# Optimization experiments

Hardware: AMD Instinct MI355X
Metric: run time of the kernel (lower is better)

Reference implementation:

```python
import jax, jax.numpy as jnp
import numpy as np
from jax import lax

NGTH = 15  # num_gth_mem
EPS = 1e-5  # BatchNorm eps


def _conv(x, w, b):
    y = lax.conv_general_dilated(x, w, (1, 1), 'VALID',
                                 dimension_numbers=('NCHW', 'OIHW', 'NCHW'))
    return y + b[None, :, None, None]


def _bn(x, g, b, m, v):
    # eval-mode BatchNorm2d with running stats
    return g[None, :, None, None] * (x - m[None, :, None, None]) * lax.rsqrt(v[None, :, None, None] + EPS) + b[None, :, None, None]


def _masked_stats(x, w):
    # x: (B, M, ...) ; w: (B, M) float weights. Population mean/std over masked mem slots.
    extra = (1,) * (x.ndim - 2)
    we = w.reshape(w.shape[:2] + extra)
    cnt = jnp.sum(w, axis=1).reshape((w.shape[0],) + extra)
    s = jnp.sum(x * we, axis=1)
    ss = jnp.sum(x * x * we, axis=1)
    mean = s / cnt
    var = jnp.maximum(ss / cnt - mean * mean, 0.0)
    return mean, jnp.sqrt(var)


def _forward(target_scores, ptm, pmt, predicted_iou, mem_mask, params):
    nf, ns, nmem, c, h, w = ptm.shape
    B = nf * ns
    ts = target_scores.reshape(B, 1, h, w)
    pmt = pmt.reshape(B, nmem, 1, h, w)
    ptm = ptm.reshape(B, nmem, c, h, w)
    mask = mem_mask.reshape(B, nmem)
    piou = predicted_iou.reshape(B, 1, 1, 1)

    mf = mask.astype(ts.dtype)
    # rank of each selected slot within the masked (ordered) selection
    rank = jnp.cumsum(mf, axis=1) - 1.0
    gth_w = mf * (rank < NGTH).astype(ts.dtype)   # first NGTH selected slots
    oth_w = mf * (rank >= NGTH).astype(ts.dtype)  # remaining selected slots

    max_ts = jnp.max(ts.reshape(B, -1), axis=1)

    pmt_mean, pmt_std = _masked_stats(pmt, mf)                 # (B,1,h,w)
    pmt_gth = pmt[:, :NGTH]                                    # unmasked slice (as in torch code)
    pmt_gth_mean = jnp.mean(pmt_gth, axis=1)
    pmt_gth_std = jnp.std(pmt_gth, axis=1)
    pmt_oth_mean, pmt_oth_std = _masked_stats(pmt, oth_w)

    ptm_max = jnp.max(ptm.reshape(B, nmem, -1), axis=2)        # (B, nmem)
    m_mm, s_mm = _masked_stats(ptm_max, mf)
    m_gm, s_gm = _masked_stats(ptm_max, gth_w)
    m_om, s_om = _masked_stats(ptm_max, oth_w)

    def bcast(v):
        return jnp.broadcast_to(v.reshape(B, 1, 1, 1), (B, 1, h, w))

    inp = jnp.concatenate([
        bcast(max_ts), jnp.broadcast_to(piou, (B, 1, h, w)),
        pmt_mean, pmt_std, pmt_gth_mean, pmt_gth_std, pmt_oth_mean, pmt_oth_std,
        bcast(m_mm), bcast(s_mm), bcast(m_gm), bcast(s_gm), bcast(m_om), bcast(s_om)
    ], axis=1)  # (B, 14, h, w)

    (c1w, c1b, g1, b1, m1, v1, c2w, c2b, g2, b2, m2, v2,
     c3w, c3b, g3, b3, m3, v3, c4w, c4b) = params
    x = jax.nn.relu(_bn(_conv(inp, c1w, c1b), g1, b1, m1, v1))
    x = lax.reduce_window(x, -jnp.inf, lax.max, (1, 1, 2, 2), (1, 1, 2, 2), 'VALID')
    x = jax.nn.relu(_bn(_conv(x, c2w, c2b), g2, b2, m2, v2))
    x = jax.nn.relu(_bn(_conv(x, c3w, c3b), g3, b3, m3, v3))
    x = _conv(x, c4w, c4b)
    return jnp.max(x, axis=(2, 3), keepdims=True)  # AdaptiveMaxPool2d((1,1)) -> (B,1,1,1)


def setup_inputs() -> dict:
    key = jax.random.key(0)
    ks = jax.random.split(key, 16)
    nf, ns, nmem, h, w = 16, 32, 30, 32, 32
    d = {}
    d['target_scores'] = jax.random.normal(ks[0], (nf, ns, 1, h, w), jnp.float32)
    d['ptm'] = jax.random.uniform(ks[1], (nf, ns, nmem, 1, h, w), jnp.float32)
    d['pmt'] = jax.random.uniform(ks[2], (nf, ns, nmem, 1, h, w), jnp.float32)
    d['predicted_iou'] = jax.random.uniform(ks[3], (nf, ns), jnp.float32)
    mask = jax.random.uniform(ks[4], (nf, ns, nmem)) < 0.7
    mask = mask.at[..., :20].set(True)  # >= 20 selected -> 'other' set non-empty
    d['mem_mask'] = mask
    d['conv1_w'] = jax.random.normal(ks[5], (64, 14, 3, 3), jnp.float32) * 0.1
    d['conv1_b'] = jnp.zeros((64,), jnp.float32)
    d['bn1_g'] = jnp.ones((64,), jnp.float32); d['bn1_b'] = jnp.zeros((64,), jnp.float32)
    d['bn1_m'] = jnp.zeros((64,), jnp.float32); d['bn1_v'] = jnp.ones((64,), jnp.float32)
    d['conv2_w'] = jax.random.normal(ks[6], (64, 64, 3, 3), jnp.float32) * 0.05
    d['conv2_b'] = jnp.zeros((64,), jnp.float32)
    d['bn2_g'] = jnp.ones((64,), jnp.float32); d['bn2_b'] = jnp.zeros((64,), jnp.float32)
    d['bn2_m'] = jnp.zeros((64,), jnp.float32); d['bn2_v'] = jnp.ones((64,), jnp.float32)
    d['conv3_w'] = jax.random.normal(ks[7], (64, 64, 3, 3), jnp.float32) * 0.05
    d['conv3_b'] = jnp.zeros((64,), jnp.float32)
    d['bn3_g'] = jnp.ones((64,), jnp.float32); d['bn3_b'] = jnp.zeros((64,), jnp.float32)
    d['bn3_m'] = jnp.zeros((64,), jnp.float32); d['bn3_v'] = jnp.ones((64,), jnp.float32)
    d['conv4_w'] = jax.random.normal(ks[8], (1, 64, 3, 3), jnp.float32) * 0.05
    d['conv4_b'] = jnp.zeros((1,), jnp.float32)
    return d


def reference(target_scores, ptm, pmt, predicted_iou, mem_mask,
              conv1_w, conv1_b, bn1_g, bn1_b, bn1_m, bn1_v,
              conv2_w, conv2_b, bn2_g, bn2_b, bn2_m, bn2_v,
              conv3_w, conv3_b, bn3_g, bn3_b, bn3_m, bn3_v,
              conv4_w, conv4_b):
    params = (conv1_w, conv1_b, bn1_g, bn1_b, bn1_m, bn1_v,
              conv2_w, conv2_b, bn2_g, bn2_b, bn2_m, bn2_v,
              conv3_w, conv3_b, bn3_g, bn3_b, bn3_m, bn3_v,
              conv4_w, conv4_b)
    return _forward(target_scores, ptm, pmt, predicted_iou, mem_mask, params)
```

## Files before the change

kernel.cpp:

```cpp
#include <hip/hip_runtime.h>
#include <math.h>

#define NFB  512
#define NMEM 30
#define PIX  1024
#define EPSF 1e-5f

typedef _Float16 half8_t __attribute__((ext_vector_type(8)));
typedef _Float16 half4_t __attribute__((ext_vector_type(4)));
typedef float float4_t __attribute__((ext_vector_type(4)));

#define OFF_W2R   13631488
#define OFF_W3R   13705216
#define OFF_WR1   13778944
#define OFF_WSUM1 13791232

__global__ __launch_bounds__(256) void k_prep(
    const float* __restrict__ c1w, const float* __restrict__ c2w,
    const float* __restrict__ c3w, _Float16* __restrict__ w2rep,
    _Float16* __restrict__ w3rep, _Float16* __restrict__ wr1,
    float* __restrict__ wsum1)
{
  int i = blockIdx.x * 256 + threadIdx.x;
  if (i < 36864) {
    int kr = i / 12288, rem = i - kr * 12288;
    int oc = rem / 192, k = rem - oc * 192;
    int kc = k >> 6, ci = k & 63;
    w2rep[i] = (_Float16)c2w[((oc * 64 + ci) * 3 + kr) * 3 + kc];
  } else if (i < 73728) {
    int j = i - 36864;
    int kr = j / 12288, rem = j - kr * 12288;
    int oc = rem / 192, k = rem - oc * 192;
    int kc = k >> 6, ci = k & 63;
    w3rep[j] = (_Float16)c3w[((oc * 64 + ci) * 3 + kr) * 3 + kc];
  } else if (i < 79872) {
    int j = i - 73728;
    int kr = j / 2048, rem = j - kr * 2048;
    int oc = rem >> 5, k = rem & 31;
    int kc = k >> 3, ci = k & 7;
    _Float16 v = (_Float16)0.f;
    if (kc < 3 && ci < 6)
      v = (_Float16)c1w[((oc * 14 + (2 + ci)) * 3 + kr) * 3 + kc];
    wr1[j] = v;
  } else if (i < 80384) {
    int j = i - 79872;
    int oc = j >> 3, u = j & 7;
    const int uch[8] = {0, 1, 8, 9, 10, 11, 12, 13};
    const float* wp = c1w + (oc * 14 + uch[u]) * 9;
    float s = 0.f;
    #pragma unroll
    for (int k = 0; k < 9; ++k) s += wp[k];
    wsum1[j] = s;
  }
}

__global__ __launch_bounds__(256, 2) void k_mega(
    const float* __restrict__ ts, const float* __restrict__ ptm,
    const float* __restrict__ pmt, const float* __restrict__ piou,
    const int* __restrict__ mask,
    const _Float16* __restrict__ wr1, const float* __restrict__ wsum1,
    const float* __restrict__ c1b, const float* __restrict__ g1,
    const float* __restrict__ b1, const float* __restrict__ m1,
    const float* __restrict__ v1,
    const _Float16* __restrict__ w2rep,
    const float* __restrict__ c2b, const float* __restrict__ g2,
    const float* __restrict__ b2, const float* __restrict__ m2,
    const float* __restrict__ v2,
    const _Float16* __restrict__ w3rep,
    const float* __restrict__ c3b, const float* __restrict__ g3,
    const float* __restrict__ b3, const float* __restrict__ m3,
    const float* __restrict__ v3,
    const float* __restrict__ c4w, const float* __restrict__ c4b,
    _Float16* __restrict__ x2h, float* __restrict__ out)
{
  __shared__ __align__(16) char s_buf[55296];
  __shared__ float s_wm[NMEM], s_wo[NMEM], s_pmax[NMEM];
  __shared__ float s_red[4], s_scal[12], s_cnt[4];
  __shared__ float s_w4[576];

  const int b = blockIdx.x, t = threadIdx.x;
  const int lane = t & 63, wave = t >> 6;
  const int n16 = lane & 15, q = lane >> 4;
  _Float16* const IMG = (_Float16*)s_buf;
  _Float16* const X1  = (_Float16*)(s_buf + 16448);
  _Float16* const X2S = (_Float16*)s_buf;
  _Float16* const X3  = (_Float16*)(s_buf + 29952);

  for (int i = t; i < 576; i += 256) {
    int ci = i / 9, k = i - ci * 9;
    s_w4[k * 64 + ci] = c4w[i];
  }
  if (t == 0) {
    float cum = 0.f, cm = 0.f, cg = 0.f, co = 0.f;
    for (int m = 0; m < NMEM; ++m) {
      float f  = (mask[b * NMEM + m] != 0) ? 1.f : 0.f;
      float gg = (cum < 15.f) ? f : 0.f;
      float oo = f - gg;
      cum += f;
      s_wm[m] = f; s_wo[m] = oo;
      cm += f; cg += gg; co += oo;
    }
    s_cnt[0] = cm; s_cnt[1] = cg; s_cnt[2] = co;
  }
  for (int m = wave; m < NMEM; m += 4) {
    const float* p = ptm + ((size_t)b * NMEM + m) * PIX;
    float4 v0 = *(const float4*)(p + lane * 4);
    float4 v1_ = *(const float4*)(p + lane * 4 + 256);
    float4 v2_ = *(const float4*)(p + lane * 4 + 512);
    float4 v3_ = *(const float4*)(p + lane * 4 + 768);
    float mx = fmaxf(fmaxf(fmaxf(v0.x, v0.y), fmaxf(v0.z, v0.w)),
                     fmaxf(fmaxf(v1_.x, v1_.y), fmaxf(v1_.z, v1_.w)));
    mx = fmaxf(mx, fmaxf(fmaxf(fmaxf(v2_.x, v2_.y), fmaxf(v2_.z, v2_.w)),
                         fmaxf(fmaxf(v3_.x, v3_.y), fmaxf(v3_.z, v3_.w))));
    #pragma unroll
    for (int off = 32; off > 0; off >>= 1)
      mx = fmaxf(mx, __shfl_down(mx, off, 64));
    if (lane == 0) s_pmax[m] = mx;
  }
  {
    float4 v = ((const float4*)(ts + (size_t)b * PIX))[t];
    float mx = fmaxf(fmaxf(v.x, v.y), fmaxf(v.z, v.w));
    #pragma unroll
    for (int off = 32; off > 0; off >>= 1)
      mx = fmaxf(mx, __shfl_down(mx, off, 64));
    if (lane == 0) s_red[wave] = mx;
  }
  __syncthreads();
  if (t == 0) {
    float maxts = fmaxf(fmaxf(s_red[0], s_red[1]), fmaxf(s_red[2], s_red[3]));
    float sm = 0, sm2 = 0, sg = 0, sg2 = 0, so = 0, so2 = 0;
    for (int m = 0; m < NMEM; ++m) {
      float x = s_pmax[m];
      float gg = s_wm[m] - s_wo[m];
      sm += s_wm[m] * x;  sm2 += s_wm[m] * x * x;
      sg += gg * x;       sg2 += gg * x * x;
      so += s_wo[m] * x;  so2 += s_wo[m] * x * x;
    }
    float cm = s_cnt[0], cg = s_cnt[1], co = s_cnt[2];
    float a = sm / cm, g = sg / cg, o = so / co;
    s_scal[0] = maxts; s_scal[1] = piou[b];
    s_scal[2] = a; s_scal[3] = sqrtf(fmaxf(sm2 / cm - a * a, 0.f));
    s_scal[4] = g; s_scal[5] = sqrtf(fmaxf(sg2 / cg - g * g, 0.f));
    s_scal[6] = o; s_scal[7] = sqrtf(fmaxf(so2 / co - o * o, 0.f));
  }
  {
    const float cm = s_cnt[0], co = s_cnt[2];
    const int p0 = t * 4;
    const float* pb = pmt + (size_t)b * NMEM * PIX + p0;
    float sA[4] = {0,0,0,0}, qA[4] = {0,0,0,0};
    float sG[4] = {0,0,0,0}, qG[4] = {0,0,0,0};
    float sO[4] = {0,0,0,0}, qO[4] = {0,0,0,0};
    #pragma unroll 1
    for (int mb = 0; mb < 15; mb += 5) {
      float4 v[5];
      #pragma unroll
      for (int j = 0; j < 5; ++j) v[j] = *(const float4*)(pb + (size_t)(mb + j) * PIX);
      #pragma unroll
      for (int j = 0; j < 5; ++j) {
        float wm = s_wm[mb + j], wo = s_wo[mb + j];
        float xv[4] = {v[j].x, v[j].y, v[j].z, v[j].w};
        #pragma unroll
        for (int k = 0; k < 4; ++k) {
          float x = xv[k];
          sA[k] = fmaf(wm, x, sA[k]); qA[k] = fmaf(wm * x, x, qA[k]);
          sO[k] = fmaf(wo, x, sO[k]); qO[k] = fmaf(wo * x, x, qO[k]);
          sG[k] += x; qG[k] = fmaf(x, x, qG[k]);
        }
      }
    }
    #pragma unroll 1
    for (int mb = 15; mb < 30; mb += 5) {
      float4 v[5];
      #pragma unroll
      for (int j = 0; j < 5; ++j) v[j] = *(const float4*)(pb + (size_t)(mb + j) * PIX);
      #pragma unroll
      for (int j = 0; j < 5; ++j) {
        float wm = s_wm[mb + j], wo = s_wo[mb + j];
        float xv[4] = {v[j].x, v[j].y, v[j].z, v[j].w};
        #pragma unroll
        for (int k = 0; k < 4; ++k) {
          float x = xv[k];
          sA[k] = fmaf(wm, x, sA[k]); qA[k] = fmaf(wm * x, x, qA[k]);
          sO[k] = fmaf(wo, x, sO[k]); qO[k] = fmaf(wo * x, x, qO[k]);
        }
      }
    }
    half8_t* ob = (half8_t*)(IMG) + p0;
    #pragma unroll
    for (int j = 0; j < 4; ++j) {
      float m0 = sA[j] / cm;   float d0 = sqrtf(fmaxf(qA[j] / cm - m0 * m0, 0.f));
      float m1_ = sG[j] / 15.f; float d1 = sqrtf(fmaxf(qG[j] / 15.f - m1_ * m1_, 0.f));
      float m2_ = sO[j] / co;   float d2 = sqrtf(fmaxf(qO[j] / co - m2_ * m2_, 0.f));
      half8_t v;
      v[0] = (_Float16)m0;  v[1] = (_Float16)d0;
      v[2] = (_Float16)m1_; v[3] = (_Float16)d1;
      v[4] = (_Float16)m2_; v[5] = (_Float16)d2;
      v[6] = (_Float16)0.f; v[7] = (_Float16)0.f;
      ob[j] = v;
    }
    if (t < 4) {
      half8_t z = {(_Float16)0.f,(_Float16)0.f,(_Float16)0.f,(_Float16)0.f,
                   (_Float16)0.f,(_Float16)0.f,(_Float16)0.f,(_Float16)0.f};
      ((half8_t*)IMG)[1024 + t] = z;
    }
  }
  __syncthreads();

  {
    const int ocA = wave * 16 + n16;
    half8_t af[3];
    #pragma unroll
    for (int kr = 0; kr < 3; ++kr)
      af[kr] = *(const half8_t*)(wr1 + (kr * 64 + ocA) * 32 + q * 8);
    const int oc0 = wave * 16 + q * 4;
    float scv[4], shv[4], cst[4];
    #pragma unroll
    for (int rg = 0; rg < 4; ++rg) {
      int oc = oc0 + rg;
      float s = g1[oc] * rsqrtf(v1[oc] + EPSF);
      scv[rg] = s;
      shv[rg] = (c1b[oc] - m1[oc]) * s + b1[oc];
      float c = 0.f;
      #pragma unroll
      for (int u = 0; u < 8; ++u) c = fmaf(wsum1[oc * 8 + u], s_scal[u], c);
      cst[rg] = c;
    }
    #pragma unroll 1
    for (int pr = 0; pr < 15; ++pr) {
      const int r0 = pr * 2;
      float4_t acc[2][2];
      #pragma unroll
      for (int row = 0; row < 2; ++row)
        #pragma unroll
        for (int tt = 0; tt < 2; ++tt)
          acc[row][tt] = (float4_t){0.f, 0.f, 0.f, 0.f};
      #pragma unroll
      for (int row = 0; row < 2; ++row) {
        #pragma unroll
        for (int kr = 0; kr < 3; ++kr) {
          const int ip = (r0 + row + kr) * 32 + n16 + q;
          #pragma unroll
          for (int tt = 0; tt < 2; ++tt) {
            half8_t bf = *(const half8_t*)(IMG + (ip + tt * 16) * 8);
            acc[row][tt] = __builtin_amdgcn_mfma_f32_16x16x32_f16(
                af[kr], bf, acc[row][tt], 0, 0, 0);
          }
        }
      }
      #pragma unroll
      for (int tt = 0; tt < 2; ++tt) {
        float mm[4];
        #pragma unroll
        for (int j = 0; j < 4; ++j) {
          float m = fmaxf(acc[0][tt][j], acc[1][tt][j]);
          mm[j] = fmaxf(m, __shfl_xor(m, 1, 64));
        }
        if ((n16 & 1) == 0) {
          int pc = tt * 8 + (n16 >> 1);
          half4_t vv;
          if (pc < 15) {
            #pragma unroll
            for (int rg = 0; rg < 4; ++rg)
              vv[rg] = (_Float16)fmaxf(scv[rg] * (mm[rg] + cst[rg]) + shv[rg], 0.f);
          } else {
            vv[0] = (_Float16)0.f; vv[1] = (_Float16)0.f;
            vv[2] = (_Float16)0.f; vv[3] = (_Float16)0.f;
          }
          *(half4_t*)(X1 + (pr * 16 + pc) * 72 + oc0) = vv;
        }
      }
    }
  }
  __syncthreads();

  {
    int base72[11];
    #pragma unroll
    for (int nt = 0; nt < 11; ++nt) {
      int p = nt * 16 + n16;
      int pe = (p < 169) ? p : 168;
      int r = pe / 13, c = pe - r * 13;
      base72[nt] = (r * 16 + c) * 72;
    }
    float4_t acc[11];
    #pragma unroll
    for (int nt = 0; nt < 11; ++nt) acc[nt] = (float4_t){0.f, 0.f, 0.f, 0.f};
    const int ocA = wave * 16 + n16;
    #pragma unroll 1
    for (int kr = 0; kr < 3; ++kr) {
      half8_t af[6];
      const half8_t* wp = (const half8_t*)(w2rep + (size_t)(kr * 64 + ocA) * 192 + q * 8);
      #pragma unroll
      for (int ks = 0; ks < 6; ++ks) af[ks] = wp[ks * 4];
      const int krbase = kr * (16 * 72);
      #pragma unroll
      for (int ks = 0; ks < 6; ++ks) {
        const int k0 = ks * 32 + q * 8;
        const int kadd = krbase + (k0 >> 6) * 72 + (k0 & 63);
        #pragma unroll
        for (int nt = 0; nt < 11; ++nt) {
          half8_t bf = *(const half8_t*)(X1 + base72[nt] + kadd);
          acc[nt] = __builtin_amdgcn_mfma_f32_16x16x32_f16(af[ks], bf, acc[nt], 0, 0, 0);
        }
      }
    }
    const int ocb = wave * 16 + q * 4;
    float scv[4], shv[4];
    #pragma unroll
    for (int rg = 0; rg < 4; ++rg) {
      int o = ocb + rg;
      float s = g2[o] * rsqrtf(v2[o] + EPSF);
      scv[rg] = s;
      shv[rg] = (c2b[o] - m2[o]) * s + b2[o];
    }
    #pragma unroll
    for (int nt = 0; nt < 11; ++nt) {
      int p = nt * 16 + n16;
      if (p < 169) {
        int r = p / 13, c = p - r * 13;
        half4_t vv;
        #pragma unroll
        for (int rg = 0; rg < 4; ++rg)
          vv[rg] = (_Float16)fmaxf(acc[nt][rg] * scv[rg] + shv[rg], 0.f);
        *(half4_t*)(x2h + (((size_t)b * 13 + r) * 16 + c) * 64 + ocb) = vv;
      }
    }
  }
  __threadfence_block();
  __syncthreads();
  {
    const half8_t* src = (const half8_t*)(x2h + (size_t)b * 13 * 16 * 64);
    half8_t* dst = (half8_t*)X2S;
    for (int g = t; g < 208 * 8; g += 256) {
      int pix = g >> 3, cib = g & 7;
      dst[pix * 9 + cib] = src[g];
    }
  }
  __syncthreads();

  {
    int base72[8];
    #pragma unroll
    for (int nt = 0; nt < 8; ++nt) {
      int p = nt * 16 + n16;
      int pe = (p < 121) ? p : 120;
      int r = pe / 11, c = pe - r * 11;
      base72[nt] = (r * 16 + c) * 72;
    }
    float4_t acc[8];
    #pragma unroll
    for (int nt = 0; nt < 8; ++nt) acc[nt] = (float4_t){0.f, 0.f, 0.f, 0.f};
    const int ocA = wave * 16 + n16;
    #pragma unroll 1
    for (int kr = 0; kr < 3; ++kr) {
      half8_t af[6];
      const half8_t* wp = (const half8_t*)(w3rep + (size_t)(kr * 64 + ocA) * 192 + q * 8);
      #pragma unroll
      for (int ks = 0; ks < 6; ++ks) af[ks] = wp[ks * 4];
      const int krbase = kr * (16 * 72);
      #pragma unroll
      for (int ks = 0; ks < 6; ++ks) {
        const int k0 = ks * 32 + q * 8;
        const int kadd = krbase + (k0 >> 6) * 72 + (k0 & 63);
        #pragma unroll
        for (int nt = 0; nt < 8; ++nt) {
          half8_t bf = *(const half8_t*)(X2S + base72[nt] + kadd);
          acc[nt] = __builtin_amdgcn_mfma_f32_16x16x32_f16(af[ks], bf, acc[nt], 0, 0, 0);
        }
      }
    }
    const int ocb = wave * 16 + q * 4;
    float scv[4], shv[4];
    #pragma unroll
    for (int rg = 0; rg < 4; ++rg) {
      int o = ocb + rg;
      float s = g3[o] * rsqrtf(v3[o] + EPSF);
      scv[rg] = s;
      shv[rg] = (c3b[o] - m3[o]) * s + b3[o];
    }
    #pragma unroll
    for (int nt = 0; nt < 8; ++nt) {
      int p = nt * 16 + n16;
      if (p < 121) {
        int r = p / 11, c = p - r * 11;
        half4_t vv;
        #pragma unroll
        for (int rg = 0; rg < 4; ++rg)
          vv[rg] = (_Float16)fmaxf(acc[nt][rg] * scv[rg] + shv[rg], 0.f);
        *(half4_t*)(X3 + (r * 16 + c) * 72 + ocb) = vv;
      }
    }
  }
  __syncthreads();

  {
    float val = -INFINITY;
    if (t < 81) {
      const int r = t / 9, c = t - (t / 9) * 9;
      float acc = 0.f;
      #pragma unroll
      for (int kr = 0; kr < 3; ++kr)
        #pragma unroll
        for (int kc = 0; kc < 3; ++kc) {
          const _Float16* ip = X3 + ((r + kr) * 16 + (c + kc)) * 72;
          const float* wk = s_w4 + (kr * 3 + kc) * 64;
          #pragma unroll
          for (int cig = 0; cig < 8; ++cig) {
            half8_t x = *(const half8_t*)(ip + cig * 8);
            #pragma unroll
            for (int j = 0; j < 8; ++j)
              acc = fmaf((float)x[j], wk[cig * 8 + j], acc);
          }
        }
      val = acc;
    }
    #pragma unroll
    for (int off = 32; off > 0; off >>= 1)
      val = fmaxf(val, __shfl_down(val, off, 64));
    if (lane == 0) s_red[wave] = val;
    __syncthreads();
    if (t == 0)
      out[b] = fmaxf(fmaxf(s_red[0], s_red[1]), fmaxf(s_red[2], s_red[3])) + c4b[0];
  }
}

extern "C" void kernel_launch(void* const* d_in, const int* in_sizes, int n_in,
                              void* d_out, int out_size, void* d_ws, size_t ws_size,
                              hipStream_t stream) {
  const float* ts   = (const float*)d_in[0];
  const float* ptm  = (const float*)d_in[1];
  const float* pmt  = (const float*)d_in[2];
  const float* piou = (const float*)d_in[3];
  const int*   mask = (const int*)d_in[4];
  const float* c1w = (const float*)d_in[5];
  const float* c1b = (const float*)d_in[6];
  const float* g1  = (const float*)d_in[7];
  const float* b1  = (const float*)d_in[8];
  const float* m1  = (const float*)d_in[9];
  const float* v1  = (const float*)d_in[10];
  const float* c2w = (const float*)d_in[11];
  const float* c2b = (const float*)d_in[12];
  const float* g2  = (const float*)d_in[13];
  const float* b2  = (const float*)d_in[14];
  const float* m2  = (const float*)d_in[15];
  const float* v2  = (const float*)d_in[16];
  const float* c3w = (const float*)d_in[17];
  const float* c3b = (const float*)d_in[18];
  const float* g3  = (const float*)d_in[19];
  const float* b3  = (const float*)d_in[20];
  const float* m3  = (const float*)d_in[21];
  const float* v3  = (const float*)d_in[22];
  const float* c4w = (const float*)d_in[23];
  const float* c4b = (const float*)d_in[24];

  char* ws = (char*)d_ws;
  _Float16*  x2h   = (_Float16*)ws;
  _Float16*  w2rep = (_Float16*)(ws + OFF_W2R);
  _Float16*  w3rep = (_Float16*)(ws + OFF_W3R);
  _Float16*  wr1   = (_Float16*)(ws + OFF_WR1);
  float*     wsum1 = (float*)(ws + OFF_WSUM1);

  k_prep<<<314, 256, 0, stream>>>(c1w, c2w, c3w, w2rep, w3rep, wr1, wsum1);
  k_mega<<<NFB, 256, 0, stream>>>(
      ts, ptm, pmt, piou, mask,
      wr1, wsum1, c1b, g1, b1, m1, v1,
      w2rep, c2b, g2, b2, m2, v2,
      w3rep, c3b, g3, b3, m3, v3,
      c4w, c4b, x2h, (float*)d_out);
}
```

Baseline: 222.3 us.

## Keep conv2 output in LDS and batch global loads ahead of compute

The conv2 epilogue now writes its activations straight into the shared-memory buffer used by conv3. Before, it wrote them to a global scratch buffer and copied them back after a thread fence, so that global round trip goes away. A barrier is added before the write because the LDS region overlaps conv2's input. The ptm max and pmt statistics loops now issue all their global loads up front, and the conv2/conv3 weight fragments are hoisted out of the kr loop. This exposes more memory-level parallelism but raises register pressure, which under launch_bounds(256,2) risks spills.

```diff
diff --git a/kernel.cpp b/kernel.cpp
--- a/kernel.cpp
+++ b/kernel.cpp
@@ -71,7 +71,7 @@
     const float* __restrict__ b3, const float* __restrict__ m3,
     const float* __restrict__ v3,
     const float* __restrict__ c4w, const float* __restrict__ c4b,
-    _Float16* __restrict__ x2h, float* __restrict__ out)
+    float* __restrict__ out)
 {
   __shared__ __align__(16) char s_buf[55296];
   __shared__ float s_wm[NMEM], s_wo[NMEM], s_pmax[NMEM];
@@ -102,20 +102,33 @@
     }
     s_cnt[0] = cm; s_cnt[1] = cg; s_cnt[2] = co;
   }
-  for (int m = wave; m < NMEM; m += 4) {
-    const float* p = ptm + ((size_t)b * NMEM + m) * PIX;
-    float4 v0 = *(const float4*)(p + lane * 4);
-    float4 v1_ = *(const float4*)(p + lane * 4 + 256);
-    float4 v2_ = *(const float4*)(p + lane * 4 + 512);
-    float4 v3_ = *(const float4*)(p + lane * 4 + 768);
-    float mx = fmaxf(fmaxf(fmaxf(v0.x, v0.y), fmaxf(v0.z, v0.w)),
-                     fmaxf(fmaxf(v1_.x, v1_.y), fmaxf(v1_.z, v1_.w)));
-    mx = fmaxf(mx, fmaxf(fmaxf(fmaxf(v2_.x, v2_.y), fmaxf(v2_.z, v2_.w)),
-                         fmaxf(fmaxf(v3_.x, v3_.y), fmaxf(v3_.z, v3_.w))));
-    #pragma unroll
-    for (int off = 32; off > 0; off >>= 1)
-      mx = fmaxf(mx, __shfl_down(mx, off, 64));
-    if (lane == 0) s_pmax[m] = mx;
+  {
+    float4 u[8][4];
+    const float* pb = ptm + (size_t)b * NMEM * PIX + lane * 4;
+    #pragma unroll
+    for (int k = 0; k < 8; ++k) {
+      int m = wave + 4 * k;
+      if (m < NMEM) {
+        const float* p = pb + (size_t)m * PIX;
+        #pragma unroll
+        for (int j = 0; j < 4; ++j) u[k][j] = *(const float4*)(p + j * 256);
+      }
+    }
+    #pragma unroll
+    for (int k = 0; k < 8; ++k) {
+      int m = wave + 4 * k;
+      if (m < NMEM) {
+        float4 v0 = u[k][0], v1_ = u[k][1], v2_ = u[k][2], v3_ = u[k][3];
+        float mx = fmaxf(fmaxf(fmaxf(v0.x, v0.y), fmaxf(v0.z, v0.w)),
+                         fmaxf(fmaxf(v1_.x, v1_.y), fmaxf(v1_.z, v1_.w)));
+        mx = fmaxf(mx, fmaxf(fmaxf(fmaxf(v2_.x, v2_.y), fmaxf(v2_.z, v2_.w)),
+                             fmaxf(fmaxf(v3_.x, v3_.y), fmaxf(v3_.z, v3_.w))));
+        #pragma unroll
+        for (int off = 32; off > 0; off >>= 1)
+          mx = fmaxf(mx, __shfl_down(mx, off, 64));
+        if (lane == 0) s_pmax[m] = mx;
+      }
+    }
   }
   {
     float4 v = ((const float4*)(ts + (size_t)b * PIX))[t];
@@ -147,42 +160,35 @@
     const float cm = s_cnt[0], co = s_cnt[2];
     const int p0 = t * 4;
     const float* pb = pmt + (size_t)b * NMEM * PIX + p0;
+    float4 va[15], vb[15];
+    #pragma unroll
+    for (int j = 0; j < 15; ++j) va[j] = *(const float4*)(pb + (size_t)j * PIX);
+    #pragma unroll
+    for (int j = 0; j < 15; ++j) vb[j] = *(const float4*)(pb + (size_t)(15 + j) * PIX);
     float sA[4] = {0,0,0,0}, qA[4] = {0,0,0,0};
     float sG[4] = {0,0,0,0}, qG[4] = {0,0,0,0};
     float sO[4] = {0,0,0,0}, qO[4] = {0,0,0,0};
-    #pragma unroll 1
-    for (int mb = 0; mb < 15; mb += 5) {
-      float4 v[5];
-      #pragma unroll
-      for (int j = 0; j < 5; ++j) v[j] = *(const float4*)(pb + (size_t)(mb + j) * PIX);
-      #pragma unroll
-      for (int j = 0; j < 5; ++j) {
-        float wm = s_wm[mb + j], wo = s_wo[mb + j];
-        float xv[4] = {v[j].x, v[j].y, v[j].z, v[j].w};
-        #pragma unroll
-        for (int k = 0; k < 4; ++k) {
-          float x = xv[k];
-          sA[k] = fmaf(wm, x, sA[k]); qA[k] = fmaf(wm * x, x, qA[k]);
-          sO[k] = fmaf(wo, x, sO[k]); qO[k] = fmaf(wo * x, x, qO[k]);
-          sG[k] += x; qG[k] = fmaf(x, x, qG[k]);
-        }
-      }
-    }
-    #pragma unroll 1
-    for (int mb = 15; mb < 30; mb += 5) {
-      float4 v[5];
-      #pragma unroll
-      for (int j = 0; j < 5; ++j) v[j] = *(const float4*)(pb + (size_t)(mb + j) * PIX);
-      #pragma unroll
-      for (int j = 0; j < 5; ++j) {
-        float wm = s_wm[mb + j], wo = s_wo[mb + j];
-        float xv[4] = {v[j].x, v[j].y, v[j].z, v[j].w};
-        #pragma unroll
-        for (int k = 0; k < 4; ++k) {
-          float x = xv[k];
-          sA[k] = fmaf(wm, x, sA[k]); qA[k] = fmaf(wm * x, x, qA[k]);
-          sO[k] = fmaf(wo, x, sO[k]); qO[k] = fmaf(wo * x, x, qO[k]);
-        }
+    #pragma unroll
+    for (int j = 0; j < 15; ++j) {
+      float wm = s_wm[j], wo = s_wo[j];
+      float xv[4] = {va[j].x, va[j].y, va[j].z, va[j].w};
+      #pragma unroll
+      for (int k = 0; k < 4; ++k) {
+        float x = xv[k];
+        sA[k] = fmaf(wm, x, sA[k]); qA[k] = fmaf(wm * x, x, qA[k]);
+        sO[k] = fmaf(wo, x, sO[k]); qO[k] = fmaf(wo * x, x, qO[k]);
+        sG[k] += x; qG[k] = fmaf(x, x, qG[k]);
+      }
+    }
+    #pragma unroll
+    for (int j = 0; j < 15; ++j) {
+      float wm = s_wm[15 + j], wo = s_wo[15 + j];
+      float xv[4] = {vb[j].x, vb[j].y, vb[j].z, vb[j].w};
+      #pragma unroll
+      for (int k = 0; k < 4; ++k) {
+        float x = xv[k];
+        sA[k] = fmaf(wm, x, sA[k]); qA[k] = fmaf(wm * x, x, qA[k]);
+        sO[k] = fmaf(wo, x, sO[k]); qO[k] = fmaf(wo * x, x, qO[k]);
       }
     }
     half8_t* ob = (half8_t*)(IMG) + p0;
@@ -286,12 +292,15 @@
     #pragma unroll
     for (int nt = 0; nt < 11; ++nt) acc[nt] = (float4_t){0.f, 0.f, 0.f, 0.f};
     const int ocA = wave * 16 + n16;
+    half8_t af[3][6];
+    #pragma unroll
+    for (int kr = 0; kr < 3; ++kr) {
+      const half8_t* wp = (const half8_t*)(w2rep + (size_t)(kr * 64 + ocA) * 192 + q * 8);
+      #pragma unroll
+      for (int ks = 0; ks < 6; ++ks) af[kr][ks] = wp[ks * 4];
+    }
     #pragma unroll 1
     for (int kr = 0; kr < 3; ++kr) {
-      half8_t af[6];
-      const half8_t* wp = (const half8_t*)(w2rep + (size_t)(kr * 64 + ocA) * 192 + q * 8);
-      #pragma unroll
-      for (int ks = 0; ks < 6; ++ks) af[ks] = wp[ks * 4];
       const int krbase = kr * (16 * 72);
       #pragma unroll
       for (int ks = 0; ks < 6; ++ks) {
@@ -300,7 +309,7 @@
         #pragma unroll
         for (int nt = 0; nt < 11; ++nt) {
           half8_t bf = *(const half8_t*)(X1 + base72[nt] + kadd);
-          acc[nt] = __builtin_amdgcn_mfma_f32_16x16x32_f16(af[ks], bf, acc[nt], 0, 0, 0);
+          acc[nt] = __builtin_amdgcn_mfma_f32_16x16x32_f16(af[kr][ks], bf, acc[nt], 0, 0, 0);
         }
       }
     }
@@ -313,27 +322,21 @@
       scv[rg] = s;
       shv[rg] = (c2b[o] - m2[o]) * s + b2[o];
     }
+    half4_t vout[11];
+    #pragma unroll
+    for (int nt = 0; nt < 11; ++nt) {
+      #pragma unroll
+      for (int rg = 0; rg < 4; ++rg)
+        vout[nt][rg] = (_Float16)fmaxf(acc[nt][rg] * scv[rg] + shv[rg], 0.f);
+    }
+    __syncthreads();
     #pragma unroll
     for (int nt = 0; nt < 11; ++nt) {
       int p = nt * 16 + n16;
       if (p < 169) {
         int r = p / 13, c = p - r * 13;
-        half4_t vv;
-        #pragma unroll
-        for (int rg = 0; rg < 4; ++rg)
-          vv[rg] = (_Float16)fmaxf(acc[nt][rg] * scv[rg] + shv[rg], 0.f);
-        *(half4_t*)(x2h + (((size_t)b * 13 + r) * 16 + c) * 64 + ocb) = vv;
-      }
-    }
-  }
-  __threadfence_block();
-  __syncthreads();
-  {
-    const half8_t* src = (const half8_t*)(x2h + (size_t)b * 13 * 16 * 64);
-    half8_t* dst = (half8_t*)X2S;
-    for (int g = t; g < 208 * 8; g += 256) {
-      int pix = g >> 3, cib = g & 7;
-      dst[pix * 9 + cib] = src[g];
+        *(half4_t*)(X2S + (r * 16 + c) * 72 + ocb) = vout[nt];
+      }
     }
   }
   __syncthreads();
@@ -351,12 +354,15 @@
     #pragma unroll
     for (int nt = 0; nt < 8; ++nt) acc[nt] = (float4_t){0.f, 0.f, 0.f, 0.f};
     const int ocA = wave * 16 + n16;
+    half8_t af[3][6];
+    #pragma unroll
+    for (int kr = 0; kr < 3; ++kr) {
+      const half8_t* wp = (const half8_t*)(w3rep + (size_t)(kr * 64 + ocA) * 192 + q * 8);
+      #pragma unroll
+      for (int ks = 0; ks < 6; ++ks) af[kr][ks] = wp[ks * 4];
+    }
     #pragma unroll 1
     for (int kr = 0; kr < 3; ++kr) {
-      half8_t af[6];
-      const half8_t* wp = (const half8_t*)(w3rep + (size_t)(kr * 64 + ocA) * 192 + q * 8);
-      #pragma unroll
-      for (int ks = 0; ks < 6; ++ks) af[ks] = wp[ks * 4];
       const int krbase = kr * (16 * 72);
       #pragma unroll
       for (int ks = 0; ks < 6; ++ks) {
@@ -365,7 +371,7 @@
         #pragma unroll
         for (int nt = 0; nt < 8; ++nt) {
           half8_t bf = *(const half8_t*)(X2S + base72[nt] + kadd);
-          acc[nt] = __builtin_amdgcn_mfma_f32_16x16x32_f16(af[ks], bf, acc[nt], 0, 0, 0);
+          acc[nt] = __builtin_amdgcn_mfma_f32_16x16x32_f16(af[kr][ks], bf, acc[nt], 0, 0, 0);
         }
       }
     }
@@ -454,7 +460,6 @@
   const float* c4b = (const float*)d_in[24];
 
   char* ws = (char*)d_ws;
-  _Float16*  x2h   = (_Float16*)ws;
   _Float16*  w2rep = (_Float16*)(ws + OFF_W2R);
   _Float16*  w3rep = (_Float16*)(ws + OFF_W3R);
   _Float16*  wr1   = (_Float16*)(ws + OFF_WR1);
@@ -466,5 +471,5 @@
       wr1, wsum1, c1b, g1, b1, m1, v1,
       w2rep, c2b, g2, b2, m2, v2,
       w3rep, c3b, g3, b3, m3, v3,
-      c4w, c4b, x2h, (float*)d_out);
+      c4w, c4b, (float*)d_out);
 }
```

Measured after the change: 246.3 us. 10.8% more time.
